# Performance work log

Measured on AMD Instinct MI355X. Metric: run time of the kernel, lower is better.

The kernel has to match this reference:

```python
import jax, jax.numpy as jnp
import numpy as np

DIM, HEADS, WS = 256, 16, 8
B, H, W = 2, 252, 252
BN_EPS = 1e-5


def _rel_index():
    # Same construction as the torch buffer relative_position_index (64,64)
    coords = np.stack(np.meshgrid(np.arange(WS), np.arange(WS), indexing='ij'))
    flat = coords.reshape(2, -1)
    rel = (flat[:, :, None] - flat[:, None, :]).transpose(1, 2, 0).copy()
    rel[..., 0] += WS - 1
    rel[..., 1] += WS - 1
    rel[..., 0] *= 2 * WS - 1
    return jnp.asarray(rel.sum(-1))

REL_IDX = _rel_index()  # (WS*WS, WS*WS) int


def _conv(x, w, pad, groups=1):
    return jax.lax.conv_general_dilated(
        x, w, (1, 1), [(pad[0], pad[0]), (pad[1], pad[1])],
        dimension_numbers=('NCHW', 'OIHW', 'NCHW'), feature_group_count=groups)


def setup_inputs() -> dict:
    key = jax.random.key(0)
    ks = jax.random.split(key, 8)
    s = lambda k, shape, sc: jax.random.normal(k, shape, jnp.float32) * sc
    z = lambda: jnp.zeros((DIM,), jnp.float32)
    return {
        'x': s(ks[0], (B, DIM, H, W), 1.0),
        'w_qkv': s(ks[1], (3 * DIM, DIM, 1, 1), 0.05),
        'rel_bias_table': s(ks[2], ((2 * WS - 1) ** 2, HEADS), 0.02),
        'w_h': s(ks[3], (DIM, DIM, WS, 1), 0.02),
        'b_h': z(),
        'w_v': s(ks[4], (DIM, DIM, 1, WS), 0.02),
        'b_v': z(),
        'w_dw': s(ks[5], (DIM, 1, WS, WS), 0.05),
        'bn_gamma': jnp.ones((DIM,), jnp.float32),
        'bn_beta': z(),
        'bn_mean': z(),
        'bn_var': jnp.ones((DIM,), jnp.float32),
        'w_pw': s(ks[6], (DIM, DIM, 1, 1), 0.05),
    }


def reference(x, w_qkv, rel_bias_table, w_h, b_h, w_v, b_v, w_dw,
              bn_gamma, bn_beta, bn_mean, bn_var, w_pw):
    Bc, C, Hc, Wc = x.shape
    pad_h, pad_w = WS - Hc % WS, WS - Wc % WS
    xp = jnp.pad(x, ((0, 0), (0, 0), (0, pad_h), (0, pad_w)), mode='reflect')
    Hp, Wp = Hc + pad_h, Wc + pad_w
    hh, ww, d = Hp // WS, Wp // WS, C // HEADS

    qkv = _conv(xp, w_qkv, (0, 0))  # (B, 3C, Hp, Wp)
    # b (qkv h d) (hh ws1) (ww ws2) -> qkv (b hh ww) h (ws1 ws2) d
    qkv = qkv.reshape(Bc, 3, HEADS, d, hh, WS, ww, WS)
    qkv = qkv.transpose(1, 0, 4, 6, 2, 5, 7, 3).reshape(3, Bc * hh * ww, HEADS, WS * WS, d)
    q, k, v = qkv[0], qkv[1], qkv[2]

    dots = jnp.einsum('nhid,nhjd->nhij', q, k) * (d ** -0.5)
    bias = rel_bias_table[REL_IDX.reshape(-1)].reshape(WS * WS, WS * WS, HEADS)
    dots = dots + bias.transpose(2, 0, 1)[None]  # (1, h, 64, 64)
    attn = jax.nn.softmax(dots, axis=-1)
    out = jnp.einsum('nhij,nhjd->nhid', attn, v)
    # (b hh ww) h (ws1 ws2) d -> b (h d) (hh ws1) (ww ws2)
    out = out.reshape(Bc, hh, ww, HEADS, WS, WS, d)
    out = out.transpose(0, 3, 6, 1, 4, 2, 5).reshape(Bc, C, Hp, Wp)
    out = out[:, :, :Hc, :Wc]

    p1 = _conv(jnp.pad(out, ((0, 0), (0, 0), (0, 1), (0, 0)), mode='reflect'),
               w_h, (WS // 2 - 1, 0)) + b_h[None, :, None, None]
    p2 = _conv(jnp.pad(out, ((0, 0), (0, 0), (0, 0), (0, 1)), mode='reflect'),
               w_v, (0, WS // 2 - 1)) + b_v[None, :, None, None]
    y = jnp.pad(p1 + p2, ((0, 0), (0, 0), (0, 1), (0, 1)), mode='reflect')
    y = _conv(y, w_dw, ((WS - 1) // 2, (WS - 1) // 2), groups=DIM)  # depthwise
    inv = bn_gamma / jnp.sqrt(bn_var + BN_EPS)
    y = y * inv[None, :, None, None] + (bn_beta - bn_mean * inv)[None, :, None, None]
    y = _conv(y, w_pw, (0, 0))  # pointwise 1x1
    return y[:, :, :Hc, :Wc]
```

## Files before the change

kernel.cpp:

```cpp
#include <hip/hip_runtime.h>
#include <hip/hip_bf16.h>

#define HC 252
#define WC 252
#define CD 256
#define NHEADS 16

#define XP_W 264
#define XP_HW (252*264)
#define XP_CHW (256*252*264)

typedef unsigned short u16;
typedef unsigned int u32;
typedef __attribute__((ext_vector_type(8))) short bf16x8;
typedef __attribute__((ext_vector_type(4))) float f32x4;
typedef __attribute__((ext_vector_type(4))) u32 u32x4;
typedef __attribute__((ext_vector_type(2))) u32 u32x2;

#define XP_BYTES (2u * (unsigned)XP_CHW * 2u)
#define ZP_OFF   XP_BYTES
#define ZP_BYTES 409600u
#define WT_OFF   (ZP_OFF + ZP_BYTES)
#define WT_ELEMS (128*8192)
#define WPW_OFF  (WT_OFF + (unsigned)WT_ELEMS*2u)
#define WPW_ELEMS (8*8192)
#define WQ_OFF   (WPW_OFF + (unsigned)WPW_ELEMS*2u)
#define WQ_ELEMS (768*256)
#define BIAS_OFF (WQ_OFF + (unsigned)WQ_ELEMS*2u)

__device__ __forceinline__ u16 bfu(float f) {
    __hip_bfloat16 h = __float2bfloat16(f);
    return *(reinterpret_cast<u16*>(&h));
}
__device__ __forceinline__ u32 pack2(float a, float b) {
    return (u32)bfu(a) | ((u32)bfu(b) << 16);
}

__global__ __launch_bounds__(512, 2) void attn_mfma(
    const float* __restrict__ x, const u16* __restrict__ WQ,
    const float* __restrict__ BIASF, u16* __restrict__ xp)
{
    __shared__ __align__(16) char smem[131072];

    const int blk = blockIdx.x;
    const int wx = blk & 31, wy = (blk >> 5) & 31, b = blk >> 10;
    const int tid = threadIdx.x;
    const int lane = tid & 63, wid = tid >> 6;
    const int g = lane >> 4, li = lane & 15;

    {
        int ci = tid >> 1;
        int rbase = (tid & 1) * 4;
        const float* srcc = x + (size_t)(b * 256 + ci) * (HC * WC);
        #pragma unroll
        for (int rr = 0; rr < 4; ++rr) {
            int r = rbase + rr;
            int h = wy * 8 + r; if (h >= HC) h = 2 * HC - 2 - h;
            const float* src = srcc + h * WC;
            float v[8];
            if (wx == 31) {
                #pragma unroll
                for (int c = 0; c < 8; ++c) {
                    int w = 248 + c; if (w >= WC) w = 2 * WC - 2 - w;
                    v[c] = src[w];
                }
            } else {
                float4 f0 = *(const float4*)(src + wx * 8);
                float4 f1 = *(const float4*)(src + wx * 8 + 4);
                v[0]=f0.x; v[1]=f0.y; v[2]=f0.z; v[3]=f0.w;
                v[4]=f1.x; v[5]=f1.y; v[6]=f1.z; v[7]=f1.w;
            }
            #pragma unroll
            for (int c = 0; c < 8; ++c) {
                int pos = r * 8 + c;
                int byte = pos * 512 + ((ci * 2) ^ ((pos & 7) << 4));
                *(u16*)(smem + byte) = bfu(v[c]);
            }
        }
    }
    __syncthreads();

    const int QKVB = 32768 + wid * 12288;

    f32x4 acc[6][4];
    #pragma unroll
    for (int m = 0; m < 6; ++m)
        #pragma unroll
        for (int nf = 0; nf < 4; ++nf) acc[m][nf] = (f32x4){0.f,0.f,0.f,0.f};

    for (int ks = 0; ks < 8; ++ks) {
        bf16x8 bx[4];
        #pragma unroll
        for (int nf = 0; nf < 4; ++nf) {
            int pos = 16 * nf + li;
            int byte = pos * 512 + ((ks * 64 + 16 * g) ^ ((pos & 7) << 4));
            bx[nf] = *(const bf16x8*)(smem + byte);
        }
        #pragma unroll
        for (int m = 0; m < 6; ++m) {
            int p = m >> 1, hh2 = m & 1;
            int o = p * 256 + 32 * wid + 16 * hh2 + li;
            bf16x8 aw = *(const bf16x8*)(WQ + o * 256 + ks * 32 + 8 * g);
            #pragma unroll
            for (int nf = 0; nf < 4; ++nf)
                acc[m][nf] = __builtin_amdgcn_mfma_f32_16x16x32_bf16(aw, bx[nf], acc[m][nf], 0, 0, 0);
        }
    }
    __syncthreads();

    #pragma unroll
    for (int m = 0; m < 6; ++m) {
        int p = m >> 1, hh2 = m & 1;
        if (p < 2) {
            char* base = smem + QKVB + p * 4096 + hh2 * 2048;
            #pragma unroll
            for (int nf = 0; nf < 4; ++nf) {
                int pos = 16 * nf + li;
                u32 lo = pack2(acc[m][nf][0], acc[m][nf][1]);
                u32 hi = pack2(acc[m][nf][2], acc[m][nf][3]);
                int byte = pos * 32 + ((8 * g) ^ (((pos >> 2) & 1) << 4));
                *(u32x2*)(base + byte) = (u32x2){lo, hi};
            }
        } else {
            char* base = smem + QKVB + 8192 + hh2 * 2048;
            #pragma unroll
            for (int nf = 0; nf < 4; ++nf) {
                int pos = 16 * nf + li;
                #pragma unroll
                for (int r = 0; r < 4; ++r) {
                    int d = 4 * g + r;
                    int byte = (pos >> 3) * 256 + d * 16 + (pos & 7) * 2;
                    *(u16*)(base + byte) = bfu(acc[m][nf][r]);
                }
            }
        }
    }

    const bf16x8 zf = {0,0,0,0,0,0,0,0};

    for (int hh2 = 0; hh2 < 2; ++hh2) {
        const int head = 2 * wid + hh2;
        const char* Qb = smem + QKVB + hh2 * 2048;
        const char* Kb = smem + QKVB + 4096 + hh2 * 2048;
        const char* Vb = smem + QKVB + 8192 + hh2 * 2048;
        char* Pb = smem + wid * 4096;

        f32x4 s[4][4];
        #pragma unroll
        for (int mf = 0; mf < 4; ++mf)
            #pragma unroll
            for (int nf = 0; nf < 4; ++nf) s[mf][nf] = (f32x4){0.f,0.f,0.f,0.f};
        bf16x8 bk[4];
        #pragma unroll
        for (int nf = 0; nf < 4; ++nf) {
            int pos = 16 * nf + li;
            bk[nf] = (g < 2) ? *(const bf16x8*)(Kb + pos * 32 + ((16 * g) ^ (((pos >> 2) & 1) << 4))) : zf;
        }
        #pragma unroll
        for (int mf = 0; mf < 4; ++mf) {
            int pos = 16 * mf + li;
            bf16x8 aq = (g < 2) ? *(const bf16x8*)(Qb + pos * 32 + ((16 * g) ^ (((pos >> 2) & 1) << 4))) : zf;
            #pragma unroll
            for (int nf = 0; nf < 4; ++nf)
                s[mf][nf] = __builtin_amdgcn_mfma_f32_16x16x32_bf16(aq, bk[nf], s[mf][nf], 0, 0, 0);
        }

        f32x4 e[4][4];
        f32x4 rs[4];
        #pragma unroll
        for (int mf = 0; mf < 4; ++mf) rs[mf] = (f32x4){0.f,0.f,0.f,0.f};
        #pragma unroll
        for (int mf = 0; mf < 4; ++mf)
            #pragma unroll
            for (int nf = 0; nf < 4; ++nf) {
                f32x4 b4 = *(const f32x4*)(BIASF + (((head * 4 + mf) * 4 + nf) * 64 + lane) * 4);
                #pragma unroll
                for (int r = 0; r < 4; ++r) {
                    float ev = __expf(s[mf][nf][r] * 0.25f + b4[r]);
                    e[mf][nf][r] = ev;
                    rs[mf][r] += ev;
                }
            }
        #pragma unroll
        for (int mf = 0; mf < 4; ++mf)
            #pragma unroll
            for (int r = 0; r < 4; ++r) {
                float t = rs[mf][r];
                t += __shfl_xor(t, 1); t += __shfl_xor(t, 2);
                t += __shfl_xor(t, 4); t += __shfl_xor(t, 8);
                rs[mf][r] = t;
            }

        f32x4 o[4];
        #pragma unroll
        for (int mf = 0; mf < 4; ++mf) o[mf] = (f32x4){0.f,0.f,0.f,0.f};
        const bool even = !(lane & 1);
        #pragma unroll
        for (int hf = 0; hf < 2; ++hf) {
            #pragma unroll
            for (int mf = 0; mf < 4; ++mf)
                #pragma unroll
                for (int nfl = 0; nfl < 2; ++nfl) {
                    f32x4 ee = e[mf][2 * hf + nfl];
                    float p0 = __shfl_xor(ee[0], 1), p1 = __shfl_xor(ee[1], 1);
                    float p2 = __shfl_xor(ee[2], 1), p3 = __shfl_xor(ee[3], 1);
                    int jl = 16 * nfl + (li & ~1);
                    u32 w0, w1; int r0;
                    if (even) { w0 = pack2(ee[0], p0); w1 = pack2(ee[1], p1); r0 = 0; }
                    else      { w0 = pack2(p2, ee[2]); w1 = pack2(p3, ee[3]); r0 = 2; }
                    int i0 = 16 * mf + 4 * g + r0, i1 = i0 + 1;
                    *(u32*)(Pb + i0 * 64 + ((2 * jl) ^ ((i0 & 3) << 4))) = w0;
                    *(u32*)(Pb + i1 * 64 + ((2 * jl) ^ ((i1 & 3) << 4))) = w1;
                }
            bf16x8 bv = *(const bf16x8*)(Vb + (4 * hf + g) * 256 + li * 16);
            #pragma unroll
            for (int mf = 0; mf < 4; ++mf) {
                int i = 16 * mf + li;
                bf16x8 ap = *(const bf16x8*)(Pb + i * 64 + ((16 * g) ^ ((i & 3) << 4)));
                o[mf] = __builtin_amdgcn_mfma_f32_16x16x32_bf16(ap, bv, o[mf], 0, 0, 0);
            }
        }

        #pragma unroll
        for (int mf = 0; mf < 4; ++mf) {
            int h = wy * 8 + 2 * mf + (g >> 1);
            int wbase = wx * 8 + 4 * (g & 1);
            if (h < HC && wbase < WC) {
                float v0 = o[mf][0] / rs[mf][0], v1 = o[mf][1] / rs[mf][1];
                float v2 = o[mf][2] / rs[mf][2], v3 = o[mf][3] / rs[mf][3];
                size_t idx = ((size_t)(b * 256 + head * 16 + li) * HC + h) * XP_W + wbase + 4;
                *(u32x2*)(xp + idx) = (u32x2){pack2(v0, v1), pack2(v2, v3)};
            }
        }
    }
}

__global__ __launch_bounds__(256) void wprep_kernel(
    const float* __restrict__ wh, const float* __restrict__ wv,
    const float* __restrict__ wpw, const float* __restrict__ wqkv,
    const float* __restrict__ btab, u16* __restrict__ wsu)
{
    int i = blockIdx.x * 256 + threadIdx.x;
    u16* WT = wsu + WT_OFF / 2;
    u16* WP = wsu + WPW_OFF / 2;
    u16* ZP = wsu + ZP_OFF / 2;
    u16* WQp = wsu + WQ_OFF / 2;
    float* BF = (float*)(wsu + BIAS_OFF / 2);
    if (i < WT_ELEMS) {
        int j = i & 7, co = (i >> 3) & 255, kb = (i >> 11) & 3, s = i >> 13;
        float v = (s < 64) ? wh[co * 2048 + s * 32 + kb * 8 + j]
                           : wv[co * 2048 + (s - 64) * 32 + kb * 8 + j];
        WT[i] = bfu(v);
    } else if (i < WT_ELEMS + WPW_ELEMS) {
        int i2 = i - WT_ELEMS;
        int j = i2 & 7, co = (i2 >> 3) & 255, kb = (i2 >> 11) & 3, s = i2 >> 13;
        WP[i2] = bfu(wpw[co * 256 + s * 32 + kb * 8 + j]);
    } else if (i < WT_ELEMS + WPW_ELEMS + (int)(ZP_BYTES / 2)) {
        ZP[i - WT_ELEMS - WPW_ELEMS] = 0;
    } else if (i < WT_ELEMS + WPW_ELEMS + (int)(ZP_BYTES / 2) + WQ_ELEMS) {
        int i4 = i - WT_ELEMS - WPW_ELEMS - (int)(ZP_BYTES / 2);
        WQp[i4] = bfu(wqkv[i4]);
    } else {
        int i5 = i - WT_ELEMS - WPW_ELEMS - (int)(ZP_BYTES / 2) - WQ_ELEMS;
        if (i5 < 16384) {
            int lane = i5 & 63, nf = (i5 >> 6) & 3, mf = (i5 >> 8) & 3, head = i5 >> 10;
            int gg = lane >> 4, ll = lane & 15;
            #pragma unroll
            for (int r = 0; r < 4; ++r) {
                int row = 16 * mf + 4 * gg + r;
                int col = 16 * nf + ll;
                int dy = (row >> 3) - (col >> 3) + 7;
                int dx = (row & 7) - (col & 7) + 7;
                BF[i5 * 4 + r] = btab[(dy * 15 + dx) * NHEADS + head];
            }
        }
    }
}

__global__ __launch_bounds__(256) void halo_kernel(u16* __restrict__ xp)
{
    int i = blockIdx.x * 256 + threadIdx.x;
    if (i >= 129024 * 12) return;
    int row = i / 12, c = i % 12;
    int wp = (c < 4) ? c : 252 + c;
    u16 v = 0;
    if (wp == 256) v = xp[row * XP_W + 254];
    xp[row * XP_W + wp] = v;
}

__global__ __launch_bounds__(512, 2) void sepconv_mfma(
    const u16* __restrict__ xp, const u16* __restrict__ WT,
    const u16* __restrict__ ZP,
    const float* __restrict__ b_h, const float* __restrict__ b_v,
    float* __restrict__ P)
{
    __shared__ u16 As[2][8192];
    __shared__ u16 Bs[2][256 * 36];

    const int bid = blockIdx.x;
    const int zz = (bid & 7) * 63 + (bid >> 3);
    const int h = zz % HC, b = zz / HC;
    const int tid = threadIdx.x;
    const int lane = tid & 63, wid = tid >> 6;
    const int wr = wid >> 2, wc = wid & 3;
    const int cq = lane & 15, kb = lane >> 4;

    const int wl2 = (tid & 127) * 2;
    const int oc = tid >> 7;

    const u16* hcur[8];
    int hstep[8];
    #pragma unroll
    for (int t = 0; t < 8; ++t) {
        int j = h + t - 3;
        bool valid = (j >= 0 && j <= 252);
        int jr = (j == 252) ? 250 : j;
        hcur[t] = valid ? (xp + (size_t)b * XP_CHW + (size_t)jr * XP_W) : ZP;
        hstep[t] = valid ? 4 * XP_HW : 0;
    }
    const u16* vbase = xp + (size_t)b * XP_CHW + (size_t)h * XP_W;
    const int hvoff = oc * XP_HW + wl2 + 4;

    const int bw0 = wl2 * 36 + oc * 8;
    const int bw1 = bw0 + 36;

    f32x4 acc[8][4];
    #pragma unroll
    for (int m = 0; m < 8; ++m)
        #pragma unroll
        for (int n = 0; n < 4; ++n) acc[m][n] = (f32x4){0.f, 0.f, 0.f, 0.f};

    u32x4 rA[2];
    u32 rB[8];

    int aw0, aw1;
    {
        int c0 = tid, c1 = 512 + tid;
        aw0 = ((c0 >> 8) * 256 + ((c0 & 255) ^ (((c0 >> 8) & 3) << 1))) * 8;
        aw1 = ((c1 >> 8) * 256 + ((c1 & 255) ^ (((c1 >> 8) & 3) << 1))) * 8;
    }

    rA[0] = *(const u32x4*)(WT + (size_t)tid * 8);
    rA[1] = *(const u32x4*)(WT + (size_t)(512 + tid) * 8);
    #pragma unroll
    for (int t = 0; t < 8; ++t)
        rB[t] = *(const u32*)(hcur[t] + hvoff);
    *(u32x4*)&As[0][aw0] = rA[0];
    *(u32x4*)&As[0][aw1] = rA[1];
    {
        union { bf16x8 v; u32 u[4]; } p0, p1;
        #pragma unroll
        for (int q = 0; q < 4; ++q) {
            p0.u[q] = __builtin_amdgcn_perm(rB[2 * q + 1], rB[2 * q], 0x05040100u);
            p1.u[q] = __builtin_amdgcn_perm(rB[2 * q + 1], rB[2 * q], 0x07060302u);
        }
        *(bf16x8*)&Bs[0][bw0] = p0.v;
        *(bf16x8*)&Bs[0][bw1] = p1.v;
    }

    for (int s = 0; s < 128; ++s) {
        const int cur = s & 1;
        const int s1 = s + 1;
        const bool hph1 = (s1 < 64);
        if (s1 < 128) {
            rA[0] = *(const u32x4*)(WT + (size_t)s1 * 8192 + (size_t)tid * 8);
            rA[1] = *(const u32x4*)(WT + (size_t)s1 * 8192 + (size_t)(512 + tid) * 8);
            if (hph1) {
                #pragma unroll
                for (int t = 0; t < 8; ++t) hcur[t] += hstep[t];
                #pragma unroll
                for (int t = 0; t < 8; ++t)
                    rB[t] = *(const u32*)(hcur[t] + hvoff);
            } else {
                int off = ((s1 - 64) * 4 + oc) * XP_HW + wl2;
                #pragma unroll
                for (int l = 0; l < 6; ++l)
                    rB[l] = *(const u32*)(vbase + off + 2 * l);
            }
        }
        __syncthreads();

        bf16x8 af[8], bfr[4];
        #pragma unroll
        for (int m = 0; m < 8; ++m) {
            int row = wr * 128 + m * 16 + cq;
            af[m] = *(const bf16x8*)&As[cur][(kb * 256 + (row ^ (kb << 1))) * 8];
        }
        #pragma unroll
        for (int n = 0; n < 4; ++n)
            bfr[n] = *(const bf16x8*)&Bs[cur][(wc * 64 + n * 16 + cq) * 36 + kb * 8];
        #pragma unroll
        for (int m = 0; m < 8; ++m)
            #pragma unroll
            for (int n = 0; n < 4; ++n)
                acc[m][n] = __builtin_amdgcn_mfma_f32_16x16x32_bf16(af[m], bfr[n], acc[m][n], 0, 0, 0);

        if (s1 < 128) {
            const int nxt = cur ^ 1;
            *(u32x4*)&As[nxt][aw0] = rA[0];
            *(u32x4*)&As[nxt][aw1] = rA[1];
            union { bf16x8 v; u32 u[4]; } p0, p1;
            if (hph1) {
                #pragma unroll
                for (int q = 0; q < 4; ++q) {
                    p0.u[q] = __builtin_amdgcn_perm(rB[2 * q + 1], rB[2 * q], 0x05040100u);
                    p1.u[q] = __builtin_amdgcn_perm(rB[2 * q + 1], rB[2 * q], 0x07060302u);
                }
            } else {
                #pragma unroll
                for (int q = 0; q < 4; ++q)
                    p0.u[q] = __builtin_amdgcn_alignbit(rB[q + 1], rB[q], 16);
                p1.u[0] = rB[1]; p1.u[1] = rB[2];
                p1.u[2] = rB[3]; p1.u[3] = rB[4];
            }
            *(bf16x8*)&Bs[nxt][bw0] = p0.v;
            *(bf16x8*)&Bs[nxt][bw1] = p1.v;
        }
    }

    const int rq = lane >> 4, cc = lane & 15;
    #pragma unroll
    for (int m = 0; m < 8; ++m) {
        int cgb = wr * 128 + m * 16 + rq * 4;
        float bias[4];
        #pragma unroll
        for (int rr = 0; rr < 4; ++rr) bias[rr] = b_h[cgb + rr] + b_v[cgb + rr];
        #pragma unroll
        for (int n = 0; n < 4; ++n) {
            int wg = wc * 64 + n * 16 + cc;
            if (wg < WC) {
                #pragma unroll
                for (int rr = 0; rr < 4; ++rr)
                    P[((size_t)(b * CD + cgb + rr) * HC + h) * WC + wg] = acc[m][n][rr] + bias[rr];
            }
        }
    }
}

__global__ __launch_bounds__(256) void dwbn_kernel(
    const float* __restrict__ P, const float* __restrict__ w_dw,
    const float* __restrict__ gamma, const float* __restrict__ beta,
    const float* __restrict__ mean, const float* __restrict__ var,
    __hip_bfloat16* __restrict__ Yb)
{
    __shared__ float ps[15][42];
    __shared__ float wd[64];
    const int bw = blockIdx.x, bh = blockIdx.y, bz = blockIdx.z;
    const int b = bz >> 8, c = bz & 255;
    const int h0 = bh * 8, w0 = bw * 32;
    const int tid = threadIdx.x;
    if (tid < 64) wd[tid] = w_dw[c * 64 + tid];
    for (int it = 0; it < 3; ++it) {
        int flat = tid + it * 256;
        if (flat < 630) {
            int row = flat / 42, col = flat % 42;
            int j = h0 - 3 + row, wcol = w0 - 3 + col;
            float v = 0.f;
            if (j >= 0 && j <= HC && wcol >= 0 && wcol <= WC) {
                int jr = (j == HC) ? (HC - 2) : j;
                int wr2 = (wcol == WC) ? (WC - 2) : wcol;
                v = P[((b * CD + c) * HC + jr) * WC + wr2];
            }
            ps[row][col] = v;
        }
    }
    __syncthreads();
    const int r = tid >> 5, cc = tid & 31;
    const int h = h0 + r, w = w0 + cc;
    if (h < HC && w < WC) {
        float s = 0.f;
        #pragma unroll
        for (int u = 0; u < 8; ++u)
            #pragma unroll
            for (int v2 = 0; v2 < 8; ++v2)
                s += wd[u * 8 + v2] * ps[r + u][cc + v2];
        const float inv = gamma[c] * rsqrtf(var[c] + 1e-5f);
        Yb[((b * CD + c) * HC + h) * WC + w] = __float2bfloat16(s * inv + (beta[c] - mean[c] * inv));
    }
}

__global__ __launch_bounds__(512, 2) void pw_mfma(
    const u16* __restrict__ Y, const u16* __restrict__ WP,
    float* __restrict__ O)
{
    __shared__ u16 As[2][8192];
    __shared__ u16 Bs[2][256 * 36];

    const int bid = blockIdx.x;
    const int zz = (bid & 7) * 63 + (bid >> 3);
    const int h = zz % HC, b = zz / HC;
    const int tid = threadIdx.x;
    const int lane = tid & 63, wid = tid >> 6;
    const int wr = wid >> 2, wc = wid & 3;
    const int cq = lane & 15, kb = lane >> 4;

    const int wl2 = (tid & 127) * 2;
    const int oc = tid >> 7;

    const u16* yb = Y + ((size_t)(b * 256 + oc * 8) * HC + h) * WC + wl2;

    const int bw0 = wl2 * 36 + oc * 8;
    const int bw1 = bw0 + 36;

    f32x4 acc[8][4];
    #pragma unroll
    for (int m = 0; m < 8; ++m)
        #pragma unroll
        for (int n = 0; n < 4; ++n) acc[m][n] = (f32x4){0.f, 0.f, 0.f, 0.f};

    u32x4 rA[2];
    u32 rB[8];

    int aw0, aw1;
    {
        int c0 = tid, c1 = 512 + tid;
        aw0 = ((c0 >> 8) * 256 + ((c0 & 255) ^ (((c0 >> 8) & 3) << 1))) * 8;
        aw1 = ((c1 >> 8) * 256 + ((c1 & 255) ^ (((c1 >> 8) & 3) << 1))) * 8;
    }

    rA[0] = *(const u32x4*)(WP + (size_t)tid * 8);
    rA[1] = *(const u32x4*)(WP + (size_t)(512 + tid) * 8);
    #pragma unroll
    for (int j = 0; j < 8; ++j)
        rB[j] = *(const u32*)(yb + (size_t)j * (HC * WC));
    *(u32x4*)&As[0][aw0] = rA[0];
    *(u32x4*)&As[0][aw1] = rA[1];
    {
        union { bf16x8 v; u32 u[4]; } p0, p1;
        #pragma unroll
        for (int q = 0; q < 4; ++q) {
            p0.u[q] = __builtin_amdgcn_perm(rB[2 * q + 1], rB[2 * q], 0x05040100u);
            p1.u[q] = __builtin_amdgcn_perm(rB[2 * q + 1], rB[2 * q], 0x07060302u);
        }
        *(bf16x8*)&Bs[0][bw0] = p0.v;
        *(bf16x8*)&Bs[0][bw1] = p1.v;
    }

    for (int s = 0; s < 8; ++s) {
        const int cur = s & 1;
        const int s1 = s + 1;
        if (s1 < 8) {
            rA[0] = *(const u32x4*)(WP + (size_t)s1 * 8192 + (size_t)tid * 8);
            rA[1] = *(const u32x4*)(WP + (size_t)s1 * 8192 + (size_t)(512 + tid) * 8);
            #pragma unroll
            for (int j = 0; j < 8; ++j)
                rB[j] = *(const u32*)(yb + (size_t)(s1 * 32 + j) * (HC * WC));
        }
        __syncthreads();

        bf16x8 af[8], bfr[4];
        #pragma unroll
        for (int m = 0; m < 8; ++m) {
            int row = wr * 128 + m * 16 + cq;
            af[m] = *(const bf16x8*)&As[cur][(kb * 256 + (row ^ (kb << 1))) * 8];
        }
        #pragma unroll
        for (int n = 0; n < 4; ++n)
            bfr[n] = *(const bf16x8*)&Bs[cur][(wc * 64 + n * 16 + cq) * 36 + kb * 8];
        #pragma unroll
        for (int m = 0; m < 8; ++m)
            #pragma unroll
            for (int n = 0; n < 4; ++n)
                acc[m][n] = __builtin_amdgcn_mfma_f32_16x16x32_bf16(af[m], bfr[n], acc[m][n], 0, 0, 0);

        if (s1 < 8) {
            const int nxt = cur ^ 1;
            *(u32x4*)&As[nxt][aw0] = rA[0];
            *(u32x4*)&As[nxt][aw1] = rA[1];
            union { bf16x8 v; u32 u[4]; } p0, p1;
            #pragma unroll
            for (int q = 0; q < 4; ++q) {
                p0.u[q] = __builtin_amdgcn_perm(rB[2 * q + 1], rB[2 * q], 0x05040100u);
                p1.u[q] = __builtin_amdgcn_perm(rB[2 * q + 1], rB[2 * q], 0x07060302u);
            }
            *(bf16x8*)&Bs[nxt][bw0] = p0.v;
            *(bf16x8*)&Bs[nxt][bw1] = p1.v;
        }
    }

    const int rq = lane >> 4, cc = lane & 15;
    #pragma unroll
    for (int m = 0; m < 8; ++m) {
        int cgb = wr * 128 + m * 16 + rq * 4;
        #pragma unroll
        for (int n = 0; n < 4; ++n) {
            int wg = wc * 64 + n * 16 + cc;
            if (wg < WC) {
                #pragma unroll
                for (int rr = 0; rr < 4; ++rr)
                    O[((size_t)(b * CD + cgb + rr) * HC + h) * WC + wg] = acc[m][n][rr];
            }
        }
    }
}

extern "C" void kernel_launch(void* const* d_in, const int* in_sizes, int n_in,
                              void* d_out, int out_size, void* d_ws, size_t ws_size,
                              hipStream_t stream)
{
    const float* x      = (const float*)d_in[0];
    const float* w_qkv  = (const float*)d_in[1];
    const float* bias_t = (const float*)d_in[2];
    const float* w_h    = (const float*)d_in[3];
    const float* b_h    = (const float*)d_in[4];
    const float* w_v    = (const float*)d_in[5];
    const float* b_v    = (const float*)d_in[6];
    const float* w_dw   = (const float*)d_in[7];
    const float* bn_g   = (const float*)d_in[8];
    const float* bn_b   = (const float*)d_in[9];
    const float* bn_m   = (const float*)d_in[10];
    const float* bn_v   = (const float*)d_in[11];
    const float* w_pw   = (const float*)d_in[12];
    float* out = (float*)d_out;

    u16* wsu = (u16*)d_ws;
    const u16* XPu = wsu;
    const u16* ZPu = wsu + ZP_OFF / 2;
    const u16* WTu = wsu + WT_OFF / 2;
    const u16* WPu = wsu + WPW_OFF / 2;
    const u16* WQu = wsu + WQ_OFF / 2;
    const float* BFu = (const float*)(wsu + BIAS_OFF / 2);

    wprep_kernel<<<5984, 256, 0, stream>>>(w_h, w_v, w_pw, w_qkv, bias_t, wsu);
    attn_mfma<<<2048, 512, 0, stream>>>(x, WQu, BFu, wsu);
    halo_kernel<<<6048, 256, 0, stream>>>(wsu);
    sepconv_mfma<<<504, 512, 0, stream>>>(XPu, WTu, ZPu, b_h, b_v, out);
    dwbn_kernel<<<dim3(8, 32, 512), 256, 0, stream>>>(out, w_dw, bn_g, bn_b, bn_m, bn_v,
                                                      (__hip_bfloat16*)d_ws);
    pw_mfma<<<504, 512, 0, stream>>>(wsu, WPu, out);
}
```

Baseline: 769.9 us.

## Shrink attention blocks to 4 waves, fusing per-head QKV projection with attention

The attention kernel now runs 256 threads per block instead of 512, and each wave handles 4 heads instead of 2. For each head it computes the QKV projection into a small per-wave LDS region and runs attention right away, rather than projecting all heads up front. This cuts LDS from 128KB to 72KB and lowers accumulator register pressure, so more blocks can be resident per CU. It also remaps block IDs with a stride-8 swizzle and raises wave priority around the MFMA sections. The cost is that each thread loads twice as many input rows, and the weight loads now sit inside the per-head loop.

```diff
diff --git a/kernel.cpp b/kernel.cpp
--- a/kernel.cpp
+++ b/kernel.cpp
@@ -36,25 +36,24 @@
     return (u32)bfu(a) | ((u32)bfu(b) << 16);
 }
 
-__global__ __launch_bounds__(512, 2) void attn_mfma(
+__global__ __launch_bounds__(256, 2) void attn_mfma(
     const float* __restrict__ x, const u16* __restrict__ WQ,
     const float* __restrict__ BIASF, u16* __restrict__ xp)
 {
-    __shared__ __align__(16) char smem[131072];
-
-    const int blk = blockIdx.x;
-    const int wx = blk & 31, wy = (blk >> 5) & 31, b = blk >> 10;
+    __shared__ __align__(16) char smem[73728];
+
+    const int bid = blockIdx.x;
+    const int zz = (bid & 7) * 256 + (bid >> 3);
+    const int wx = zz & 31, wy = (zz >> 5) & 31, b = zz >> 10;
     const int tid = threadIdx.x;
     const int lane = tid & 63, wid = tid >> 6;
     const int g = lane >> 4, li = lane & 15;
 
     {
-        int ci = tid >> 1;
-        int rbase = (tid & 1) * 4;
+        int ci = tid;
         const float* srcc = x + (size_t)(b * 256 + ci) * (HC * WC);
         #pragma unroll
-        for (int rr = 0; rr < 4; ++rr) {
-            int r = rbase + rr;
+        for (int r = 0; r < 8; ++r) {
             int h = wy * 8 + r; if (h >= HC) h = 2 * HC - 2 - h;
             const float* src = srcc + h * WC;
             float v[8];
@@ -80,70 +79,72 @@
     }
     __syncthreads();
 
-    const int QKVB = 32768 + wid * 12288;
-
-    f32x4 acc[6][4];
-    #pragma unroll
-    for (int m = 0; m < 6; ++m)
-        #pragma unroll
-        for (int nf = 0; nf < 4; ++nf) acc[m][nf] = (f32x4){0.f,0.f,0.f,0.f};
-
-    for (int ks = 0; ks < 8; ++ks) {
-        bf16x8 bx[4];
-        #pragma unroll
-        for (int nf = 0; nf < 4; ++nf) {
-            int pos = 16 * nf + li;
-            int byte = pos * 512 + ((ks * 64 + 16 * g) ^ ((pos & 7) << 4));
-            bx[nf] = *(const bf16x8*)(smem + byte);
-        }
-        #pragma unroll
-        for (int m = 0; m < 6; ++m) {
-            int p = m >> 1, hh2 = m & 1;
-            int o = p * 256 + 32 * wid + 16 * hh2 + li;
-            bf16x8 aw = *(const bf16x8*)(WQ + o * 256 + ks * 32 + 8 * g);
-            #pragma unroll
-            for (int nf = 0; nf < 4; ++nf)
-                acc[m][nf] = __builtin_amdgcn_mfma_f32_16x16x32_bf16(aw, bx[nf], acc[m][nf], 0, 0, 0);
-        }
-    }
-    __syncthreads();
-
-    #pragma unroll
-    for (int m = 0; m < 6; ++m) {
-        int p = m >> 1, hh2 = m & 1;
-        if (p < 2) {
-            char* base = smem + QKVB + p * 4096 + hh2 * 2048;
+    const int WB = 32768 + wid * 10240;
+    char* Qb = smem + WB;
+    char* Kb = smem + WB + 2048;
+    char* Vb = smem + WB + 4096;
+    char* Pb = smem + WB + 6144;
+
+    const bf16x8 zf = {0,0,0,0,0,0,0,0};
+
+    #pragma unroll 1
+    for (int hh = 0; hh < 4; ++hh) {
+        const int head = wid * 4 + hh;
+
+        f32x4 acc[3][4];
+        #pragma unroll
+        for (int p = 0; p < 3; ++p)
+            #pragma unroll
+            for (int nf = 0; nf < 4; ++nf) acc[p][nf] = (f32x4){0.f,0.f,0.f,0.f};
+
+        for (int ks = 0; ks < 8; ++ks) {
+            bf16x8 bx[4];
             #pragma unroll
             for (int nf = 0; nf < 4; ++nf) {
                 int pos = 16 * nf + li;
-                u32 lo = pack2(acc[m][nf][0], acc[m][nf][1]);
-                u32 hi = pack2(acc[m][nf][2], acc[m][nf][3]);
-                int byte = pos * 32 + ((8 * g) ^ (((pos >> 2) & 1) << 4));
-                *(u32x2*)(base + byte) = (u32x2){lo, hi};
-            }
-        } else {
-            char* base = smem + QKVB + 8192 + hh2 * 2048;
-            #pragma unroll
-            for (int nf = 0; nf < 4; ++nf) {
-                int pos = 16 * nf + li;
-                #pragma unroll
-                for (int r = 0; r < 4; ++r) {
-                    int d = 4 * g + r;
-                    int byte = (pos >> 3) * 256 + d * 16 + (pos & 7) * 2;
-                    *(u16*)(base + byte) = bfu(acc[m][nf][r]);
+                int byte = pos * 512 + ((ks * 64 + 16 * g) ^ ((pos & 7) << 4));
+                bx[nf] = *(const bf16x8*)(smem + byte);
+            }
+            bf16x8 aw[3];
+            #pragma unroll
+            for (int p = 0; p < 3; ++p) {
+                int o = p * 256 + head * 16 + li;
+                aw[p] = *(const bf16x8*)(WQ + o * 256 + ks * 32 + 8 * g);
+            }
+            __builtin_amdgcn_s_setprio(1);
+            #pragma unroll
+            for (int p = 0; p < 3; ++p)
+                #pragma unroll
+                for (int nf = 0; nf < 4; ++nf)
+                    acc[p][nf] = __builtin_amdgcn_mfma_f32_16x16x32_bf16(aw[p], bx[nf], acc[p][nf], 0, 0, 0);
+            __builtin_amdgcn_s_setprio(0);
+        }
+
+        #pragma unroll
+        for (int p = 0; p < 3; ++p) {
+            if (p < 2) {
+                char* base = (p == 0) ? Qb : Kb;
+                #pragma unroll
+                for (int nf = 0; nf < 4; ++nf) {
+                    int pos = 16 * nf + li;
+                    u32 lo = pack2(acc[p][nf][0], acc[p][nf][1]);
+                    u32 hi = pack2(acc[p][nf][2], acc[p][nf][3]);
+                    int byte = pos * 32 + ((8 * g) ^ (((pos >> 2) & 1) << 4));
+                    *(u32x2*)(base + byte) = (u32x2){lo, hi};
                 }
-            }
-        }
-    }
-
-    const bf16x8 zf = {0,0,0,0,0,0,0,0};
-
-    for (int hh2 = 0; hh2 < 2; ++hh2) {
-        const int head = 2 * wid + hh2;
-        const char* Qb = smem + QKVB + hh2 * 2048;
-        const char* Kb = smem + QKVB + 4096 + hh2 * 2048;
-        const char* Vb = smem + QKVB + 8192 + hh2 * 2048;
-        char* Pb = smem + wid * 4096;
+            } else {
+                #pragma unroll
+                for (int nf = 0; nf < 4; ++nf) {
+                    int pos = 16 * nf + li;
+                    #pragma unroll
+                    for (int r = 0; r < 4; ++r) {
+                        int d = 4 * g + r;
+                        int byte = (pos >> 3) * 256 + d * 16 + (pos & 7) * 2;
+                        *(u16*)(Vb + byte) = bfu(acc[p][nf][r]);
+                    }
+                }
+            }
+        }
 
         f32x4 s[4][4];
         #pragma unroll
@@ -156,6 +157,7 @@
             int pos = 16 * nf + li;
             bk[nf] = (g < 2) ? *(const bf16x8*)(Kb + pos * 32 + ((16 * g) ^ (((pos >> 2) & 1) << 4))) : zf;
         }
+        __builtin_amdgcn_s_setprio(1);
         #pragma unroll
         for (int mf = 0; mf < 4; ++mf) {
             int pos = 16 * mf + li;
@@ -164,6 +166,7 @@
             for (int nf = 0; nf < 4; ++nf)
                 s[mf][nf] = __builtin_amdgcn_mfma_f32_16x16x32_bf16(aq, bk[nf], s[mf][nf], 0, 0, 0);
         }
+        __builtin_amdgcn_s_setprio(0);
 
         f32x4 e[4][4];
         f32x4 rs[4];
@@ -213,12 +216,14 @@
                     *(u32*)(Pb + i1 * 64 + ((2 * jl) ^ ((i1 & 3) << 4))) = w1;
                 }
             bf16x8 bv = *(const bf16x8*)(Vb + (4 * hf + g) * 256 + li * 16);
+            __builtin_amdgcn_s_setprio(1);
             #pragma unroll
             for (int mf = 0; mf < 4; ++mf) {
                 int i = 16 * mf + li;
                 bf16x8 ap = *(const bf16x8*)(Pb + i * 64 + ((16 * g) ^ ((i & 3) << 4)));
                 o[mf] = __builtin_amdgcn_mfma_f32_16x16x32_bf16(ap, bv, o[mf], 0, 0, 0);
             }
+            __builtin_amdgcn_s_setprio(0);
         }
 
         #pragma unroll
@@ -622,7 +627,7 @@
     const float* BFu = (const float*)(wsu + BIAS_OFF / 2);
 
     wprep_kernel<<<5984, 256, 0, stream>>>(w_h, w_v, w_pw, w_qkv, bias_t, wsu);
-    attn_mfma<<<2048, 512, 0, stream>>>(x, WQu, BFu, wsu);
+    attn_mfma<<<2048, 256, 0, stream>>>(x, WQu, BFu, wsu);
     halo_kernel<<<6048, 256, 0, stream>>>(wsu);
     sepconv_mfma<<<504, 512, 0, stream>>>(XPu, WTu, ZPu, b_h, b_v, out);
     dwbn_kernel<<<dim3(8, 32, 512), 256, 0, stream>>>(out, w_dw, bn_g, bn_b, bn_m, bn_v,
```

After: 677.1 us. 1.14x faster.
